# Optimization experiments

Hardware: AMD Instinct MI355X
Metric: run time of the kernel (lower is better)

## Reference

```python
import jax, jax.numpy as jnp
import numpy as np
from math import sqrt

B, L, S = 4, 2048, 2048
D_MODEL, H = 1024, 16
E = D_MODEL // H  # head dim = 64


def setup_inputs() -> dict:
    key = jax.random.key(0)
    ks = jax.random.split(key, 11)
    s = 1.0 / sqrt(D_MODEL)
    return {
        "queries": jax.random.normal(ks[0], (B, L, D_MODEL), jnp.float32),
        "keys": jax.random.normal(ks[1], (B, S, D_MODEL), jnp.float32),
        "values": jax.random.normal(ks[2], (B, S, D_MODEL), jnp.float32),
        "Wq": jax.random.normal(ks[3], (D_MODEL, D_MODEL), jnp.float32) * s,
        "bq": jax.random.normal(ks[4], (D_MODEL,), jnp.float32) * s,
        "Wk": jax.random.normal(ks[5], (D_MODEL, D_MODEL), jnp.float32) * s,
        "bk": jax.random.normal(ks[6], (D_MODEL,), jnp.float32) * s,
        "Wv": jax.random.normal(ks[7], (D_MODEL, D_MODEL), jnp.float32) * s,
        "bv": jax.random.normal(ks[8], (D_MODEL,), jnp.float32) * s,
        "Wo": jax.random.normal(ks[9], (D_MODEL, D_MODEL), jnp.float32) * s,
        "bo": jax.random.normal(ks[10], (D_MODEL,), jnp.float32) * s,
    }


def reference(queries, keys, values, Wq, bq, Wk, bk, Wv, bv, Wo, bo):
    # QKV projections, split heads: [B, L/S, H, E]
    q = (queries @ Wq + bq).reshape(B, L, H, E)
    k = (keys @ Wk + bk).reshape(B, S, H, E)
    v = (values @ Wv + bv).reshape(B, S, H, E)
    scale = 1.0 / sqrt(E)
    scores = jnp.einsum('blhe,bshe->bhls', q, k)  # [B,H,L,S]
    A = jax.nn.softmax(scale * scores, axis=-1)   # dropout is identity in eval
    out = jnp.einsum('bhls,bshd->blhd', A, v).reshape(B, L, H * E)
    return out @ Wo + bo
```

## Files before the change

### kernel.cpp

```cpp
#include <hip/hip_runtime.h>
#include <hip/hip_bf16.h>

typedef unsigned short u16;
typedef unsigned int u32;
using short8 = __attribute__((ext_vector_type(8))) short;
using f32x4  = __attribute__((ext_vector_type(4))) float;
using f32x16 = __attribute__((ext_vector_type(16))) float;
using u32x2  = __attribute__((ext_vector_type(2))) unsigned int;
using u32x4  = __attribute__((ext_vector_type(4))) unsigned int;

#define B_  4
#define L_  2048
#define S_  2048
#define DM  1024
#define H_  16
#define E_  64

__device__ __forceinline__ u16 f2bf(float f) {
  union { float f; unsigned u; } v; v.f = f;
  unsigned u = v.u;
  unsigned r = (u + 0x7fffu + ((u >> 16) & 1u)) >> 16;
  return (u16)r;
}

__device__ __forceinline__ float exp2a(float x) {
  float r; asm("v_exp_f32 %0, %1" : "=v"(r) : "v"(x)); return r;
}

__device__ __forceinline__ u32 cvtpk(float lo, float hi) {
  u32 r; asm("v_cvt_pk_bf16_f32 %0, %1, %2" : "=v"(r) : "v"(lo), "v"(hi));
  return r;
}

__device__ __forceinline__ f32x4 mfma16(short8 a, short8 b, f32x4 c) {
  return __builtin_amdgcn_mfma_f32_16x16x32_bf16(a, b, c, 0, 0, 0);
}

__device__ __forceinline__ f32x16 mfma32(short8 a, short8 b, f32x16 c) {
  return __builtin_amdgcn_mfma_f32_32x32x16_bf16(a, b, c, 0, 0, 0);
}

__device__ __forceinline__ void gload_lds16(const u16* g, u16* l) {
  __builtin_amdgcn_global_load_lds(
      (const __attribute__((address_space(1))) unsigned int*)(const void*)g,
      (__attribute__((address_space(3))) unsigned int*)(void*)l, 16, 0, 0);
}

__global__ __launch_bounds__(256) void transp_all(const float* __restrict__ w0,
                                                  const float* __restrict__ w1,
                                                  const float* __restrict__ w2,
                                                  const float* __restrict__ w3,
                                                  u16* __restrict__ t0,
                                                  u16* __restrict__ t1,
                                                  u16* __restrict__ t2,
                                                  u16* __restrict__ t3) {
  const float* W = blockIdx.z == 0 ? w0 : blockIdx.z == 1 ? w1 :
                   blockIdx.z == 2 ? w2 : w3;
  u16* Wt = blockIdx.z == 0 ? t0 : blockIdx.z == 1 ? t1 :
            blockIdx.z == 2 ? t2 : t3;
  __shared__ float t[32][33];
  int tx = threadIdx.x & 31, ty = (threadIdx.x >> 5) & 7;
#pragma unroll
  for (int j = 0; j < 32; j += 8)
    t[ty + j][tx] = W[(size_t)(blockIdx.y * 32 + ty + j) * DM + blockIdx.x * 32 + tx];
  __syncthreads();
#pragma unroll
  for (int j = 0; j < 32; j += 8)
    Wt[(size_t)(blockIdx.x * 32 + ty + j) * DM + blockIdx.y * 32 + tx] = f2bf(t[tx][ty + j]);
}

template <int EPI>
__device__ __forceinline__ void gemm_body(const float* __restrict__ A,
                                          const u16* __restrict__ Bt,
                                          const float* __restrict__ bias,
                                          void* __restrict__ Cout,
                                          int M, int N, int K, float oscale,
                                          int bx, int by) {
  __shared__ u16 lA[128 * 32];
  __shared__ u16 lB[128 * 32];
  const int tid = threadIdx.x, wid = tid >> 6, lane = tid & 63;
  const int lr = lane & 15, lh = lane >> 4;
  const int m0 = by * 128, n0 = bx * 128;
  const int wr = wid >> 1, wc = wid & 1;

  f32x4 acc[4][4];
#pragma unroll
  for (int m = 0; m < 4; m++)
#pragma unroll
    for (int n = 0; n < 4; n++) acc[m][n] = (f32x4){0.f, 0.f, 0.f, 0.f};

  const int srow = wid * 16 + (lane >> 2);
  const int scol = (lane & 3) * 8;

  const float* a0p = A + (size_t)(m0 + srow) * K + scol;
  const float* a1p = A + (size_t)(m0 + 64 + srow) * K + scol;

  f32x4 r00 = *(const f32x4*)a0p;
  f32x4 r01 = *(const f32x4*)(a0p + 4);
  f32x4 r10 = *(const f32x4*)a1p;
  f32x4 r11 = *(const f32x4*)(a1p + 4);

  for (int k0 = 0; k0 < K; k0 += 32) {
    u32x4 w0 = {cvtpk(r00.x, r00.y), cvtpk(r00.z, r00.w),
                cvtpk(r01.x, r01.y), cvtpk(r01.z, r01.w)};
    u32x4 w1 = {cvtpk(r10.x, r10.y), cvtpk(r10.z, r10.w),
                cvtpk(r11.x, r11.y), cvtpk(r11.z, r11.w)};
    *(u32x4*)(lA + (size_t)srow * 32 + scol) = w0;
    *(u32x4*)(lA + (size_t)(64 + srow) * 32 + scol) = w1;
    gload_lds16(Bt + (size_t)(n0 + srow) * K + k0 + scol, lB + (wid * 16) * 32);
    gload_lds16(Bt + (size_t)(n0 + 64 + srow) * K + k0 + scol, lB + (64 + wid * 16) * 32);
    if (k0 + 32 < K) {
      r00 = *(const f32x4*)(a0p + k0 + 32);
      r01 = *(const f32x4*)(a0p + k0 + 36);
      r10 = *(const f32x4*)(a1p + k0 + 32);
      r11 = *(const f32x4*)(a1p + k0 + 36);
    }
    __syncthreads();
    short8 af[4], bf[4];
#pragma unroll
    for (int m = 0; m < 4; m++)
      af[m] = *(const short8*)(lA + (wr * 64 + m * 16 + lr) * 32 + lh * 8);
#pragma unroll
    for (int n = 0; n < 4; n++)
      bf[n] = *(const short8*)(lB + (wc * 64 + n * 16 + lr) * 32 + lh * 8);
#pragma unroll
    for (int m = 0; m < 4; m++)
#pragma unroll
      for (int n = 0; n < 4; n++) acc[m][n] = mfma16(af[m], bf[n], acc[m][n]);
    __syncthreads();
  }

#pragma unroll
  for (int m = 0; m < 4; m++) {
    int grow0 = m0 + wr * 64 + m * 16 + lh * 4;
#pragma unroll
    for (int n = 0; n < 4; n++) {
      int gcol = n0 + wc * 64 + n * 16 + lr;
      float bi = bias[gcol];
      float v0 = (acc[m][n][0] + bi) * oscale;
      float v1 = (acc[m][n][1] + bi) * oscale;
      float v2 = (acc[m][n][2] + bi) * oscale;
      float v3 = (acc[m][n][3] + bi) * oscale;
      if constexpr (EPI == 2) {
        float* C = (float*)Cout;
        C[(size_t)(grow0 + 0) * N + gcol] = v0;
        C[(size_t)(grow0 + 1) * N + gcol] = v1;
        C[(size_t)(grow0 + 2) * N + gcol] = v2;
        C[(size_t)(grow0 + 3) * N + gcol] = v3;
      } else {
        u32 p01 = cvtpk(v0, v1), p23 = cvtpk(v2, v3);
        u16* C = (u16*)Cout;
#pragma unroll
        for (int r = 0; r < 4; r++) {
          u32 pk = r < 2 ? p01 : p23;
          u16 bv = (r & 1) ? (u16)(pk >> 16) : (u16)(pk & 0xffff);
          int grow = grow0 + r;
          if constexpr (EPI == 0) {
            C[(size_t)grow * N + gcol] = bv;
          } else {
            int bb = grow >> 11, sl = grow & 2047;
            C[((size_t)(bb * DM) + gcol) * S_ + sl] = bv;
          }
        }
      }
    }
  }
}

__device__ __forceinline__ void gemm_body_bf16(const u16* __restrict__ A,
                                               const u16* __restrict__ Bt,
                                               const float* __restrict__ bias,
                                               float* __restrict__ Cout,
                                               int M, int N, int K,
                                               int bx, int by) {
  __shared__ u16 lA[128 * 32];
  __shared__ u16 lB[128 * 32];
  const int tid = threadIdx.x, wid = tid >> 6, lane = tid & 63;
  const int lr = lane & 15, lh = lane >> 4;
  const int m0 = by * 128, n0 = bx * 128;
  const int wr = wid >> 1, wc = wid & 1;

  f32x4 acc[4][4];
#pragma unroll
  for (int m = 0; m < 4; m++)
#pragma unroll
    for (int n = 0; n < 4; n++) acc[m][n] = (f32x4){0.f, 0.f, 0.f, 0.f};

  const int srow = wid * 16 + (lane >> 2);
  const int scol = (lane & 3) * 8;

  for (int k0 = 0; k0 < K; k0 += 32) {
#pragma unroll
    for (int p = 0; p < 2; p++) {
      int r = p * 64 + srow;
      gload_lds16(A + (size_t)(m0 + r) * K + k0 + scol, lA + (p * 64 + wid * 16) * 32);
      gload_lds16(Bt + (size_t)(n0 + r) * K + k0 + scol, lB + (p * 64 + wid * 16) * 32);
    }
    __syncthreads();
    short8 af[4], bf[4];
#pragma unroll
    for (int m = 0; m < 4; m++)
      af[m] = *(const short8*)(lA + (wr * 64 + m * 16 + lr) * 32 + lh * 8);
#pragma unroll
    for (int n = 0; n < 4; n++)
      bf[n] = *(const short8*)(lB + (wc * 64 + n * 16 + lr) * 32 + lh * 8);
#pragma unroll
    for (int m = 0; m < 4; m++)
#pragma unroll
      for (int n = 0; n < 4; n++) acc[m][n] = mfma16(af[m], bf[n], acc[m][n]);
    __syncthreads();
  }

#pragma unroll
  for (int m = 0; m < 4; m++) {
    int grow0 = m0 + wr * 64 + m * 16 + lh * 4;
#pragma unroll
    for (int n = 0; n < 4; n++) {
      int gcol = n0 + wc * 64 + n * 16 + lr;
      float bi = bias[gcol];
#pragma unroll
      for (int r = 0; r < 4; r++)
        Cout[(size_t)(grow0 + r) * N + gcol] = acc[m][n][r] + bi;
    }
  }
}

__global__ __launch_bounds__(256) void gemm_qkv(
    const float* __restrict__ q, const float* __restrict__ k, const float* __restrict__ v,
    const u16* __restrict__ WqT, const u16* __restrict__ WkT, const u16* __restrict__ WvT,
    const float* __restrict__ bq, const float* __restrict__ bk, const float* __restrict__ bv,
    u16* __restrict__ Qp, u16* __restrict__ Kp, u16* __restrict__ Vt, float qsc) {
  int lin = blockIdx.x;
  int swz = (lin & 7) * 192 + (lin >> 3);
  const int bx = swz & 7, by = (swz >> 3) & 63, z = swz >> 9;
  if (z == 0)
    gemm_body<0>(q, WqT, bq, Qp, B_ * L_, DM, DM, qsc, bx, by);
  else if (z == 1)
    gemm_body<0>(k, WkT, bk, Kp, B_ * L_, DM, DM, 1.0f, bx, by);
  else
    gemm_body<1>(v, WvT, bv, Vt, B_ * L_, DM, DM, 1.0f, bx, by);
}

__global__ __launch_bounds__(256) void gemm_out(const u16* __restrict__ A,
                                                const u16* __restrict__ Bt,
                                                const float* __restrict__ bias,
                                                float* __restrict__ C) {
  int lin = blockIdx.x;
  int swz = (lin & 7) * 64 + (lin >> 3);
  const int bx = swz & 7, by = swz >> 3;
  gemm_body_bf16(A, Bt, bias, C, B_ * L_, DM, DM, bx, by);
}

__global__ __launch_bounds__(512) void attn(const u16* __restrict__ Q,
                                            const u16* __restrict__ Kp,
                                            const u16* __restrict__ Vt,
                                            u16* __restrict__ O) {
  __shared__ u16 lK[2][64 * 64];
  __shared__ u16 lV[2][64 * 64];
  const int tid = threadIdx.x, wid = tid >> 6, lane = tid & 63;
  const int l31 = lane & 31, hi = lane >> 5;

  int lin = blockIdx.x;
  int swz = (lin & 7) * 64 + (lin >> 3);
  const int bh = swz >> 3, q0 = (swz & 7) * 256;
  const int b = bh >> 4, h = bh & 15;
  const int qrow = q0 + wid * 32 + l31;

  const u16* Qb = Q + ((size_t)(b * L_ + qrow)) * DM + h * E_ + hi * 8;
  short8 qf[4];
#pragma unroll
  for (int s = 0; s < 4; s++) qf[s] = *(const short8*)(Qb + s * 16);

  f32x16 o[2];
#pragma unroll
  for (int et = 0; et < 2; et++)
#pragma unroll
    for (int r = 0; r < 16; r++) o[et][r] = 0.f;
  float m_r = -3.0e38f, l_r = 0.f;

  const u16* Kb = Kp + ((size_t)(b * S_)) * DM + h * E_;
  const u16* Vb = Vt + ((size_t)(b * DM + h * E_)) * S_;

  const int srow = wid * 8 + (lane >> 3);
  const u16* srcK = Kb + (size_t)srow * DM + ((lane & 7) ^ (srow & 7)) * 8;
  const u16* srcV = Vb + (size_t)srow * S_ + ((lane & 7) ^ (srow & 7)) * 8;

  const int sxk = (l31 & 7) * 8;
  const int hi4 = hi * 4, hi8 = hi * 8;

  auto stage = [&](int buf, int kb) {
    gload_lds16(srcK + (size_t)kb * DM, lK[buf] + wid * 512);
    gload_lds16(srcV + kb, lV[buf] + wid * 512);
  };

  stage(0, 0);
  const int NT = S_ / 64;
  for (int it = 0; it < NT; ++it) {
    const int buf = it & 1;
    __syncthreads();
    if (it + 1 < NT) stage(buf ^ 1, (it + 1) * 64);

    f32x16 sc[2];
    const u16* kbase = lK[buf] + l31 * 64;
    __builtin_amdgcn_s_setprio(1);
#pragma unroll
    for (int kt = 0; kt < 2; kt++) {
      f32x16 a;
#pragma unroll
      for (int r = 0; r < 16; r++) a[r] = 0.f;
#pragma unroll
      for (int s = 0; s < 4; s++) {
        short8 kf = *(const short8*)(kbase + kt * 2048 + ((s * 16 + hi8) ^ sxk));
        a = mfma32(kf, qf[s], a);
      }
      sc[kt] = a;
    }
    __builtin_amdgcn_s_setprio(0);

    f32x16 mA;
#pragma unroll
    for (int r = 0; r < 16; r++) mA[r] = fmaxf(sc[0][r], sc[1][r]);
#pragma unroll
    for (int r = 0; r < 8; r++) mA[r] = fmaxf(mA[r], mA[r + 8]);
#pragma unroll
    for (int r = 0; r < 4; r++) mA[r] = fmaxf(mA[r], mA[r + 4]);
    float tm = fmaxf(fmaxf(mA[0], mA[1]), fmaxf(mA[2], mA[3]));
    tm = fmaxf(tm, __shfl_xor(tm, 32));

    if (__any(tm > m_r + 8.f)) {
      float mn = fmaxf(m_r, tm);
      float al = exp2a(m_r - mn);
      m_r = mn;
      l_r *= al;
#pragma unroll
      for (int et = 0; et < 2; et++)
#pragma unroll
        for (int r = 0; r < 16; r++) o[et][r] *= al;
    }

    u32 wp[2][8];
    float rs = 0.f;
#pragma unroll
    for (int kt = 0; kt < 2; kt++)
#pragma unroll
      for (int i = 0; i < 8; i++) {
        float p0 = exp2a(sc[kt][2 * i] - m_r);
        float p1 = exp2a(sc[kt][2 * i + 1] - m_r);
        rs += p0 + p1;
        wp[kt][i] = cvtpk(p0, p1);
      }
    rs += __shfl_xor(rs, 32);
    l_r += rs;

    __builtin_amdgcn_s_setprio(1);
#pragma unroll
    for (int et = 0; et < 2; et++) {
      const u16* vp = lV[buf] + (et * 32 + l31) * 64;
#pragma unroll
      for (int kt = 0; kt < 2; kt++)
#pragma unroll
        for (int su = 0; su < 2; su++) {
          int koff = kt * 32 + su * 16 + hi4;
          u32x2 lo = *(const u32x2*)(vp + (koff ^ sxk));
          u32x2 hp = *(const u32x2*)(vp + ((koff + 8) ^ sxk));
          u32x4 vv = {lo.x, lo.y, hp.x, hp.y};
          u32x4 pv = {wp[kt][su * 4 + 0], wp[kt][su * 4 + 1],
                      wp[kt][su * 4 + 2], wp[kt][su * 4 + 3]};
          o[et] = mfma32(*(const short8*)&vv, *(const short8*)&pv, o[et]);
        }
    }
    __builtin_amdgcn_s_setprio(0);
  }

  float inv = 1.f / l_r;
  u16* Ob = O + ((size_t)(b * L_ + qrow)) * DM + h * E_;
#pragma unroll
  for (int et = 0; et < 2; et++)
#pragma unroll
    for (int t = 0; t < 4; t++) {
      u32x2 pk;
      pk.x = cvtpk(o[et][4 * t] * inv, o[et][4 * t + 1] * inv);
      pk.y = cvtpk(o[et][4 * t + 2] * inv, o[et][4 * t + 3] * inv);
      *(u32x2*)(Ob + et * 32 + t * 8 + hi4) = pk;
    }
}

extern "C" void kernel_launch(void* const* d_in, const int* in_sizes, int n_in,
                              void* d_out, int out_size, void* d_ws, size_t ws_size,
                              hipStream_t stream) {
  (void)in_sizes; (void)n_in; (void)out_size; (void)ws_size;
  const float* q  = (const float*)d_in[0];
  const float* k  = (const float*)d_in[1];
  const float* v  = (const float*)d_in[2];
  const float* Wq = (const float*)d_in[3];
  const float* bq = (const float*)d_in[4];
  const float* Wk = (const float*)d_in[5];
  const float* bk = (const float*)d_in[6];
  const float* Wv = (const float*)d_in[7];
  const float* bv = (const float*)d_in[8];
  const float* Wo = (const float*)d_in[9];
  const float* bo = (const float*)d_in[10];

  char* w = (char*)d_ws;
  const size_t ACT = (size_t)B_ * L_ * DM * 2;
  const size_t WT  = (size_t)DM * DM * 2;
  u16* WqT = (u16*)w; w += WT;
  u16* WkT = (u16*)w; w += WT;
  u16* WvT = (u16*)w; w += WT;
  u16* WoT = (u16*)w; w += WT;
  u16* Qp  = (u16*)w; w += ACT;
  u16* Kp  = (u16*)w; w += ACT;
  u16* Vt  = (u16*)w; w += ACT;
  u16* At  = (u16*)w; w += ACT;

  transp_all<<<dim3(32, 32, 4), 256, 0, stream>>>(Wq, Wk, Wv, Wo, WqT, WkT, WvT, WoT);

  const float QSC = 0.125f * 1.44269504089f;
  gemm_qkv<<<dim3(1536), 256, 0, stream>>>(
      q, k, v, WqT, WkT, WvT, bq, bk, bv, Qp, Kp, Vt, QSC);

  attn<<<dim3(512), 512, 0, stream>>>(Qp, Kp, Vt, At);

  gemm_out<<<dim3(512), 256, 0, stream>>>(At, WoT, bo, (float*)d_out);
}
```

Baseline: 211.3 us.

## Software-pipeline attention: overlap next-tile QK MFMA with current softmax and PV

Restructures the attention loop so that the QK^T scores for tile t are computed before the softmax and PV of tile t-1. V now uses a triple buffer in shared memory so its tile stays live one iteration longer, while K keeps a double buffer. PV MFMAs are interleaved per kt with the exp/pack work, and the launch bounds now request 4 waves per SIMD. The aim is to hide the exp and LDS latency behind MFMA work, at the cost of more live registers for the two score sets, which may pressure occupancy.

```diff
diff --git a/kernel.cpp b/kernel.cpp
--- a/kernel.cpp
+++ b/kernel.cpp
@@ -251,12 +251,12 @@
   gemm_body_bf16(A, Bt, bias, C, B_ * L_, DM, DM, bx, by);
 }
 
-__global__ __launch_bounds__(512) void attn(const u16* __restrict__ Q,
-                                            const u16* __restrict__ Kp,
-                                            const u16* __restrict__ Vt,
-                                            u16* __restrict__ O) {
+__global__ __launch_bounds__(512, 4) void attn(const u16* __restrict__ Q,
+                                               const u16* __restrict__ Kp,
+                                               const u16* __restrict__ Vt,
+                                               u16* __restrict__ O) {
   __shared__ u16 lK[2][64 * 64];
-  __shared__ u16 lV[2][64 * 64];
+  __shared__ u16 lV[3][64 * 64];
   const int tid = threadIdx.x, wid = tid >> 6, lane = tid & 63;
   const int l31 = lane & 31, hi = lane >> 5;
 
@@ -271,11 +271,9 @@
 #pragma unroll
   for (int s = 0; s < 4; s++) qf[s] = *(const short8*)(Qb + s * 16);
 
-  f32x16 o[2];
-#pragma unroll
-  for (int et = 0; et < 2; et++)
-#pragma unroll
-    for (int r = 0; r < 16; r++) o[et][r] = 0.f;
+  f32x16 o0, o1;
+#pragma unroll
+  for (int r = 0; r < 16; r++) { o0[r] = 0.f; o1[r] = 0.f; }
   float m_r = -3.0e38f, l_r = 0.f;
 
   const u16* Kb = Kp + ((size_t)(b * S_)) * DM + h * E_;
@@ -288,20 +286,13 @@
   const int sxk = (l31 & 7) * 8;
   const int hi4 = hi * 4, hi8 = hi * 8;
 
-  auto stage = [&](int buf, int kb) {
-    gload_lds16(srcK + (size_t)kb * DM, lK[buf] + wid * 512);
-    gload_lds16(srcV + kb, lV[buf] + wid * 512);
+  auto stage = [&](int ks, int vs, int kb) {
+    gload_lds16(srcK + (size_t)kb * DM, lK[ks] + wid * 512);
+    gload_lds16(srcV + kb, lV[vs] + wid * 512);
   };
 
-  stage(0, 0);
-  const int NT = S_ / 64;
-  for (int it = 0; it < NT; ++it) {
-    const int buf = it & 1;
-    __syncthreads();
-    if (it + 1 < NT) stage(buf ^ 1, (it + 1) * 64);
-
-    f32x16 sc[2];
-    const u16* kbase = lK[buf] + l31 * 64;
+  auto qk = [&](int ks, f32x16* sc) {
+    const u16* kbase = lK[ks] + l31 * 64;
     __builtin_amdgcn_s_setprio(1);
 #pragma unroll
     for (int kt = 0; kt < 2; kt++) {
@@ -316,7 +307,9 @@
       sc[kt] = a;
     }
     __builtin_amdgcn_s_setprio(0);
-
+  };
+
+  auto smpv = [&](int vs, f32x16* sc) {
     f32x16 mA;
 #pragma unroll
     for (int r = 0; r < 16; r++) mA[r] = fmaxf(sc[0][r], sc[1][r]);
@@ -333,56 +326,77 @@
       m_r = mn;
       l_r *= al;
 #pragma unroll
-      for (int et = 0; et < 2; et++)
-#pragma unroll
-        for (int r = 0; r < 16; r++) o[et][r] *= al;
-    }
-
-    u32 wp[2][8];
+      for (int r = 0; r < 16; r++) { o0[r] *= al; o1[r] *= al; }
+    }
+
+    const u16* vp0 = lV[vs] + l31 * 64;
+    const u16* vp1 = vp0 + 2048;
     float rs = 0.f;
 #pragma unroll
-    for (int kt = 0; kt < 2; kt++)
+    for (int kt = 0; kt < 2; kt++) {
+      u32 wpk[8];
 #pragma unroll
       for (int i = 0; i < 8; i++) {
         float p0 = exp2a(sc[kt][2 * i] - m_r);
         float p1 = exp2a(sc[kt][2 * i + 1] - m_r);
         rs += p0 + p1;
-        wp[kt][i] = cvtpk(p0, p1);
+        wpk[i] = cvtpk(p0, p1);
       }
+      __builtin_amdgcn_s_setprio(1);
+#pragma unroll
+      for (int su = 0; su < 2; su++) {
+        u32x4 pw = {wpk[su * 4 + 0], wpk[su * 4 + 1],
+                    wpk[su * 4 + 2], wpk[su * 4 + 3]};
+        short8 pf = *(const short8*)&pw;
+        int ka = ((kt * 32 + su * 16 + hi4) ^ sxk);
+        int kb2 = ((kt * 32 + su * 16 + hi4 + 8) ^ sxk);
+        u32x2 lo0 = *(const u32x2*)(vp0 + ka);
+        u32x2 hp0 = *(const u32x2*)(vp0 + kb2);
+        u32x4 vv0 = {lo0.x, lo0.y, hp0.x, hp0.y};
+        o0 = mfma32(*(const short8*)&vv0, pf, o0);
+        u32x2 lo1 = *(const u32x2*)(vp1 + ka);
+        u32x2 hp1 = *(const u32x2*)(vp1 + kb2);
+        u32x4 vv1 = {lo1.x, lo1.y, hp1.x, hp1.y};
+        o1 = mfma32(*(const short8*)&vv1, pf, o1);
+      }
+      __builtin_amdgcn_s_setprio(0);
+    }
     rs += __shfl_xor(rs, 32);
     l_r += rs;
-
-    __builtin_amdgcn_s_setprio(1);
-#pragma unroll
-    for (int et = 0; et < 2; et++) {
-      const u16* vp = lV[buf] + (et * 32 + l31) * 64;
-#pragma unroll
-      for (int kt = 0; kt < 2; kt++)
-#pragma unroll
-        for (int su = 0; su < 2; su++) {
-          int koff = kt * 32 + su * 16 + hi4;
-          u32x2 lo = *(const u32x2*)(vp + (koff ^ sxk));
-          u32x2 hp = *(const u32x2*)(vp + ((koff + 8) ^ sxk));
-          u32x4 vv = {lo.x, lo.y, hp.x, hp.y};
-          u32x4 pv = {wp[kt][su * 4 + 0], wp[kt][su * 4 + 1],
-                      wp[kt][su * 4 + 2], wp[kt][su * 4 + 3]};
-          o[et] = mfma32(*(const short8*)&vv, *(const short8*)&pv, o[et]);
-        }
-    }
-    __builtin_amdgcn_s_setprio(0);
-  }
+  };
+
+  const int NT = S_ / 64;
+
+  stage(0, 0, 0);
+  __syncthreads();
+  stage(1, 1, 64);
+  f32x16 scA[2], scB[2];
+  qk(0, scA);
+
+  int vm1 = 0, v0 = 1, vp1 = 2;
+  for (int t = 1; t < NT; ++t) {
+    __syncthreads();
+    if (t + 1 < NT) stage((t + 1) & 1, vp1, (t + 1) * 64);
+    qk(t & 1, scB);
+    smpv(vm1, scA);
+#pragma unroll
+    for (int kt = 0; kt < 2; kt++) scA[kt] = scB[kt];
+    int tmp = vm1; vm1 = v0; v0 = vp1; vp1 = tmp;
+  }
+  smpv(vm1, scA);
 
   float inv = 1.f / l_r;
   u16* Ob = O + ((size_t)(b * L_ + qrow)) * DM + h * E_;
 #pragma unroll
-  for (int et = 0; et < 2; et++)
-#pragma unroll
-    for (int t = 0; t < 4; t++) {
-      u32x2 pk;
-      pk.x = cvtpk(o[et][4 * t] * inv, o[et][4 * t + 1] * inv);
-      pk.y = cvtpk(o[et][4 * t + 2] * inv, o[et][4 * t + 3] * inv);
-      *(u32x2*)(Ob + et * 32 + t * 8 + hi4) = pk;
-    }
+  for (int t = 0; t < 4; t++) {
+    u32x2 pk;
+    pk.x = cvtpk(o0[4 * t] * inv, o0[4 * t + 1] * inv);
+    pk.y = cvtpk(o0[4 * t + 2] * inv, o0[4 * t + 3] * inv);
+    *(u32x2*)(Ob + t * 8 + hi4) = pk;
+    pk.x = cvtpk(o1[4 * t] * inv, o1[4 * t + 1] * inv);
+    pk.y = cvtpk(o1[4 * t + 2] * inv, o1[4 * t + 3] * inv);
+    *(u32x2*)(Ob + 32 + t * 8 + hi4) = pk;
+  }
 }
 
 extern "C" void kernel_launch(void* const* d_in, const int* in_sizes, int n_in,
```

After: 612.0 us. +189.6%, slower.

## Use K=64 tiles with XOR-swizzled LDS in output projection GEMM

Applied to the files above, without the earlier changes.

The output projection GEMM is inlined and now stages 64-wide K tiles instead of 32, which halves the number of barrier pairs per tile. Global-to-LDS columns are XOR-swizzled by row and read back with the matching swizzle to avoid LDS bank conflicts. In the QKV GEMM the B-tile global-to-LDS loads are issued before the A conversion and stores, so they overlap that work. The unused fp32 epilogue branch is removed. LDS use per block doubles, which may lower occupancy.

```diff
diff --git a/kernel.cpp b/kernel.cpp
--- a/kernel.cpp
+++ b/kernel.cpp
@@ -101,14 +101,14 @@
   f32x4 r11 = *(const f32x4*)(a1p + 4);
 
   for (int k0 = 0; k0 < K; k0 += 32) {
+    gload_lds16(Bt + (size_t)(n0 + srow) * K + k0 + scol, lB + (wid * 16) * 32);
+    gload_lds16(Bt + (size_t)(n0 + 64 + srow) * K + k0 + scol, lB + (64 + wid * 16) * 32);
     u32x4 w0 = {cvtpk(r00.x, r00.y), cvtpk(r00.z, r00.w),
                 cvtpk(r01.x, r01.y), cvtpk(r01.z, r01.w)};
     u32x4 w1 = {cvtpk(r10.x, r10.y), cvtpk(r10.z, r10.w),
                 cvtpk(r11.x, r11.y), cvtpk(r11.z, r11.w)};
     *(u32x4*)(lA + (size_t)srow * 32 + scol) = w0;
     *(u32x4*)(lA + (size_t)(64 + srow) * 32 + scol) = w1;
-    gload_lds16(Bt + (size_t)(n0 + srow) * K + k0 + scol, lB + (wid * 16) * 32);
-    gload_lds16(Bt + (size_t)(n0 + 64 + srow) * K + k0 + scol, lB + (64 + wid * 16) * 32);
     if (k0 + 32 < K) {
       r00 = *(const f32x4*)(a0p + k0 + 32);
       r01 = *(const f32x4*)(a0p + k0 + 36);
@@ -141,86 +141,20 @@
       float v1 = (acc[m][n][1] + bi) * oscale;
       float v2 = (acc[m][n][2] + bi) * oscale;
       float v3 = (acc[m][n][3] + bi) * oscale;
-      if constexpr (EPI == 2) {
-        float* C = (float*)Cout;
-        C[(size_t)(grow0 + 0) * N + gcol] = v0;
-        C[(size_t)(grow0 + 1) * N + gcol] = v1;
-        C[(size_t)(grow0 + 2) * N + gcol] = v2;
-        C[(size_t)(grow0 + 3) * N + gcol] = v3;
-      } else {
-        u32 p01 = cvtpk(v0, v1), p23 = cvtpk(v2, v3);
-        u16* C = (u16*)Cout;
-#pragma unroll
-        for (int r = 0; r < 4; r++) {
-          u32 pk = r < 2 ? p01 : p23;
-          u16 bv = (r & 1) ? (u16)(pk >> 16) : (u16)(pk & 0xffff);
-          int grow = grow0 + r;
-          if constexpr (EPI == 0) {
-            C[(size_t)grow * N + gcol] = bv;
-          } else {
-            int bb = grow >> 11, sl = grow & 2047;
-            C[((size_t)(bb * DM) + gcol) * S_ + sl] = bv;
-          }
+      u32 p01 = cvtpk(v0, v1), p23 = cvtpk(v2, v3);
+      u16* C = (u16*)Cout;
+#pragma unroll
+      for (int r = 0; r < 4; r++) {
+        u32 pk = r < 2 ? p01 : p23;
+        u16 bv = (r & 1) ? (u16)(pk >> 16) : (u16)(pk & 0xffff);
+        int grow = grow0 + r;
+        if constexpr (EPI == 0) {
+          C[(size_t)grow * N + gcol] = bv;
+        } else {
+          int bb = grow >> 11, sl = grow & 2047;
+          C[((size_t)(bb * DM) + gcol) * S_ + sl] = bv;
         }
       }
-    }
-  }
-}
-
-__device__ __forceinline__ void gemm_body_bf16(const u16* __restrict__ A,
-                                               const u16* __restrict__ Bt,
-                                               const float* __restrict__ bias,
-                                               float* __restrict__ Cout,
-                                               int M, int N, int K,
-                                               int bx, int by) {
-  __shared__ u16 lA[128 * 32];
-  __shared__ u16 lB[128 * 32];
-  const int tid = threadIdx.x, wid = tid >> 6, lane = tid & 63;
-  const int lr = lane & 15, lh = lane >> 4;
-  const int m0 = by * 128, n0 = bx * 128;
-  const int wr = wid >> 1, wc = wid & 1;
-
-  f32x4 acc[4][4];
-#pragma unroll
-  for (int m = 0; m < 4; m++)
-#pragma unroll
-    for (int n = 0; n < 4; n++) acc[m][n] = (f32x4){0.f, 0.f, 0.f, 0.f};
-
-  const int srow = wid * 16 + (lane >> 2);
-  const int scol = (lane & 3) * 8;
-
-  for (int k0 = 0; k0 < K; k0 += 32) {
-#pragma unroll
-    for (int p = 0; p < 2; p++) {
-      int r = p * 64 + srow;
-      gload_lds16(A + (size_t)(m0 + r) * K + k0 + scol, lA + (p * 64 + wid * 16) * 32);
-      gload_lds16(Bt + (size_t)(n0 + r) * K + k0 + scol, lB + (p * 64 + wid * 16) * 32);
-    }
-    __syncthreads();
-    short8 af[4], bf[4];
-#pragma unroll
-    for (int m = 0; m < 4; m++)
-      af[m] = *(const short8*)(lA + (wr * 64 + m * 16 + lr) * 32 + lh * 8);
-#pragma unroll
-    for (int n = 0; n < 4; n++)
-      bf[n] = *(const short8*)(lB + (wc * 64 + n * 16 + lr) * 32 + lh * 8);
-#pragma unroll
-    for (int m = 0; m < 4; m++)
-#pragma unroll
-      for (int n = 0; n < 4; n++) acc[m][n] = mfma16(af[m], bf[n], acc[m][n]);
-    __syncthreads();
-  }
-
-#pragma unroll
-  for (int m = 0; m < 4; m++) {
-    int grow0 = m0 + wr * 64 + m * 16 + lh * 4;
-#pragma unroll
-    for (int n = 0; n < 4; n++) {
-      int gcol = n0 + wc * 64 + n * 16 + lr;
-      float bi = bias[gcol];
-#pragma unroll
-      for (int r = 0; r < 4; r++)
-        Cout[(size_t)(grow0 + r) * N + gcol] = acc[m][n][r] + bi;
     }
   }
 }
@@ -245,10 +179,65 @@
                                                 const u16* __restrict__ Bt,
                                                 const float* __restrict__ bias,
                                                 float* __restrict__ C) {
+  const int N = DM, K = DM;
   int lin = blockIdx.x;
   int swz = (lin & 7) * 64 + (lin >> 3);
   const int bx = swz & 7, by = swz >> 3;
-  gemm_body_bf16(A, Bt, bias, C, B_ * L_, DM, DM, bx, by);
+
+  __shared__ u16 lA[128 * 64];
+  __shared__ u16 lB[128 * 64];
+  const int tid = threadIdx.x, wid = tid >> 6, lane = tid & 63;
+  const int lr = lane & 15, lh = lane >> 4;
+  const int m0 = by * 128, n0 = bx * 128;
+  const int wr = wid >> 1, wc = wid & 1;
+
+  f32x4 acc[4][4];
+#pragma unroll
+  for (int m = 0; m < 4; m++)
+#pragma unroll
+    for (int n = 0; n < 4; n++) acc[m][n] = (f32x4){0.f, 0.f, 0.f, 0.f};
+
+  const int sr = lane >> 3;
+  const int scx = ((lane & 7) ^ (sr & 7)) * 8;
+  const int sxr = (lr & 7) * 8;
+
+  for (int k0 = 0; k0 < K; k0 += 64) {
+#pragma unroll
+    for (int p = 0; p < 4; p++) {
+      int row = wid * 32 + p * 8 + sr;
+      gload_lds16(A + (size_t)(m0 + row) * K + k0 + scx, lA + (wid * 32 + p * 8) * 64);
+      gload_lds16(Bt + (size_t)(n0 + row) * K + k0 + scx, lB + (wid * 32 + p * 8) * 64);
+    }
+    __syncthreads();
+#pragma unroll
+    for (int s = 0; s < 2; s++) {
+      short8 af[4], bf[4];
+#pragma unroll
+      for (int m = 0; m < 4; m++)
+        af[m] = *(const short8*)(lA + (wr * 64 + m * 16 + lr) * 64 + ((s * 32 + lh * 8) ^ sxr));
+#pragma unroll
+      for (int n = 0; n < 4; n++)
+        bf[n] = *(const short8*)(lB + (wc * 64 + n * 16 + lr) * 64 + ((s * 32 + lh * 8) ^ sxr));
+#pragma unroll
+      for (int m = 0; m < 4; m++)
+#pragma unroll
+        for (int n = 0; n < 4; n++) acc[m][n] = mfma16(af[m], bf[n], acc[m][n]);
+    }
+    __syncthreads();
+  }
+
+#pragma unroll
+  for (int m = 0; m < 4; m++) {
+    int grow0 = m0 + wr * 64 + m * 16 + lh * 4;
+#pragma unroll
+    for (int n = 0; n < 4; n++) {
+      int gcol = n0 + wc * 64 + n * 16 + lr;
+      float bi = bias[gcol];
+#pragma unroll
+      for (int r = 0; r < 4; r++)
+        C[(size_t)(grow0 + r) * N + gcol] = acc[m][n][r] + bi;
+    }
+  }
 }
 
 __global__ __launch_bounds__(512) void attn(const u16* __restrict__ Q,
```

After: 208.4 us, median of 2. About the same (-1.4%).
